# Optimization experiments

Hardware: AMD Instinct MI355X
Metric: run time of the kernel (lower is better)

## Reference

```python
import jax, jax.numpy as jnp
import numpy as np

# norse LIFParameters(method='super', alpha=100) defaults
DT = 0.001
TAU_SYN_INV = 200.0
TAU_MEM_INV = 100.0
V_TH = 1.0
ALPHA = 100.0  # SuperSpike surrogate slope


@jax.custom_vjp
def superspike(x):
    # Heaviside forward, SuperSpike surrogate gradient backward
    return (x > 0).astype(x.dtype)

def _ss_fwd(x):
    return (x > 0).astype(x.dtype), x

def _ss_bwd(x, g):
    return (g / (ALPHA * jnp.abs(x) + 1.0) ** 2,)

superspike.defvjp(_ss_fwd, _ss_bwd)


def setup_inputs() -> dict:
    key = jax.random.key(0)
    k0, k1, k2 = jax.random.split(key, 3)
    T, B, F = 200, 256, 28
    H1, HC, OC, NOUT = 200, 2, 4, 10
    spl1 = F * F // HC   # 392
    spl2 = H1 // OC      # 50
    x = jax.random.normal(k0, (T, B, F, F), jnp.float32)
    Wh = jax.random.normal(k1, (HC, H1, spl1), jnp.float32) / np.sqrt(spl1).astype(np.float32)
    bh = jnp.zeros((HC, H1), jnp.float32)
    Wo = jax.random.normal(k2, (OC, NOUT, spl2), jnp.float32) / np.sqrt(spl2).astype(np.float32)
    bo = jnp.zeros((OC, NOUT), jnp.float32)
    return {"x": x, "Wh": Wh, "bh": bh, "Wo": Wo, "bo": bo}


def reference(x, Wh, bh, Wo, bo):
    T, B = x.shape[0], x.shape[1]
    HC, H1, spl1 = Wh.shape           # hidden dendritic channels
    OC, NOUT, spl2 = Wo.shape         # output dendritic channels
    dtype = x.dtype
    # flatten image and pre-split into hidden dendritic channels: [T,B,HC,spl1]
    xf = x.reshape(T, B, HC * spl1).reshape(T, B, HC, spl1)

    def step(state, xt):
        vh, ih, vo, io = state
        # --- hidden LIF layer, one LIF compartment per dendritic channel ---
        cur_h = jnp.einsum('bci,coi->bco', xt, Wh) + bh           # [B,HC,H1]
        vh_dec = vh + DT * TAU_MEM_INV * (-vh + ih)               # leak + integrate
        z = superspike(vh_dec - V_TH)                             # spikes [B,HC,H1]
        vh_new = (1.0 - z) * vh_dec                               # reset to 0
        ih_new = ih * (1.0 - DT * TAU_SYN_INV) + cur_h            # synaptic current
        s = z.sum(axis=1)                                         # combine channels -> [B,H1]
        # --- output LI (non-spiking) layer over output dendritic channels ---
        so = s.reshape(B, OC, spl2)                               # split hidden spikes
        cur_o = jnp.einsum('bci,coi->bco', so, Wo) + bo           # [B,OC,10]
        vo_new = vo + DT * TAU_MEM_INV * (-vo + io)
        io_new = io * (1.0 - DT * TAU_SYN_INV) + cur_o
        v = vo_new.sum(axis=1)                                    # [B,10]
        return (vh_new, ih_new, vo_new, io_new), v

    init = (jnp.zeros((B, HC, H1), dtype), jnp.zeros((B, HC, H1), dtype),
            jnp.zeros((B, OC, NOUT), dtype), jnp.zeros((B, OC, NOUT), dtype))
    _, voltages = jax.lax.scan(step, init, xf)                    # [T,B,10]
    return voltages
```

## Files before the change

### kernel.cpp

```cpp
#include <hip/hip_runtime.h>

#define T_STEPS 200
#define BATCH   256
#define HCH     2
#define H1      200
#define SPL1    392
#define OCH     4
#define NOUTC   10
#define SPL2    50
#define M_TOTAL (T_STEPS*BATCH)


#define BM 80
#define BN 100
#define BK 8

__global__ __launch_bounds__(256)
void k1_gemm(const float* __restrict__ X, const float* __restrict__ Wh,
             const float* __restrict__ bh, float* __restrict__ CUR)
{
    __shared__ float As[BK][BM];
    __shared__ float Ws[BK][BN];
    const int tid = threadIdx.x;
    const int m0 = blockIdx.x * BM;
    const int n0 = blockIdx.y * BN;
    const int c  = blockIdx.z;

    const bool active = tid < 250;
    const int rowg = tid / 25;
    const int colg = tid % 25;

    const float* Xc = X  + (size_t)m0 * (HCH*SPL1) + c*SPL1;
    const float* Wc = Wh + (size_t)c * H1 * SPL1 + (size_t)n0 * SPL1;

    float acc[8][4];
#pragma unroll
    for (int i = 0; i < 8; ++i)
#pragma unroll
        for (int j = 0; j < 4; ++j) acc[i][j] = 0.f;

    for (int k0 = 0; k0 < SPL1; k0 += BK) {
        for (int idx = tid; idx < BM*BK; idx += 256) {
            int m = idx >> 3, k = idx & 7;
            As[k][m] = Xc[(size_t)m*(HCH*SPL1) + k0 + k];
        }
        for (int idx = tid; idx < BN*BK; idx += 256) {
            int n = idx >> 3, k = idx & 7;
            Ws[k][n] = Wc[(size_t)n*SPL1 + k0 + k];
        }
        __syncthreads();
        if (active) {
#pragma unroll
            for (int k = 0; k < BK; ++k) {
                float4 a0 = *(const float4*)&As[k][rowg*8];
                float4 a1 = *(const float4*)&As[k][rowg*8 + 4];
                float4 w  = *(const float4*)&Ws[k][colg*4];
                float av[8] = {a0.x, a0.y, a0.z, a0.w, a1.x, a1.y, a1.z, a1.w};
                float wv[4] = {w.x, w.y, w.z, w.w};
#pragma unroll
                for (int i = 0; i < 8; ++i)
#pragma unroll
                    for (int j = 0; j < 4; ++j)
                        acc[i][j] = __builtin_fmaf(av[i], wv[j], acc[i][j]);
            }
        }
        __syncthreads();
    }

    if (active) {
        const int gn = n0 + colg*4;
        float4 bias = *(const float4*)&bh[c*H1 + gn];
#pragma unroll
        for (int i = 0; i < 8; ++i) {
            size_t m = m0 + rowg*8 + i;
            float4 v;
            v.x = __fadd_rn(acc[i][0], bias.x);
            v.y = __fadd_rn(acc[i][1], bias.y);
            v.z = __fadd_rn(acc[i][2], bias.z);
            v.w = __fadd_rn(acc[i][3], bias.w);
            *(float4*)&CUR[(m*HCH + c)*H1 + gn] = v;
        }
    }
}

__global__ __launch_bounds__(256)
void k2_lif(const float* __restrict__ CUR, unsigned char* __restrict__ S)
{
    const int tid = blockIdx.x * 256 + threadIdx.x;
    const int b = tid / H1;
    const int h = tid - b*H1;
    const size_t cbase = (size_t)b*(HCH*H1) + h;
    const int    soff  = b*(OCH*52) + (h/SPL2)*52 + (h%SPL2);
    const size_t tstr  = (size_t)BATCH*HCH*H1;
    const size_t sstr  = (size_t)BATCH*OCH*52;

    float c0[8], c1[8];
#pragma unroll
    for (int p = 0; p < 8; ++p) {
        c0[p] = CUR[(size_t)p*tstr + cbase];
        c1[p] = CUR[(size_t)p*tstr + cbase + H1];
    }

    float vh0 = 0.f, ih0 = 0.f, vh1 = 0.f, ih1 = 0.f;

    for (int tb = 0; tb < T_STEPS; tb += 8) {
#pragma unroll
        for (int u = 0; u < 8; ++u) {
            const int t = tb + u;
            float cc0 = c0[u], cc1 = c1[u];
            if (t + 8 < T_STEPS) {
                c0[u] = CUR[(size_t)(t+8)*tstr + cbase];
                c1[u] = CUR[(size_t)(t+8)*tstr + cbase + H1];
            }
            float vd0 = __fadd_rn(vh0, __fmul_rn(0.1f, __fsub_rn(ih0, vh0)));
            float vd1 = __fadd_rn(vh1, __fmul_rn(0.1f, __fsub_rn(ih1, vh1)));
            int z0 = vd0 > 1.0f;
            int z1 = vd1 > 1.0f;
            vh0 = z0 ? 0.f : vd0;
            vh1 = z1 ? 0.f : vd1;
            ih0 = __fadd_rn(__fmul_rn(ih0, 0.8f), cc0);
            ih1 = __fadd_rn(__fmul_rn(ih1, 0.8f), cc1);

            S[(size_t)t*sstr + soff] = (unsigned char)(z0 + z1);
        }
    }
}

__global__ __launch_bounds__(256)
void k3_outgemm(const unsigned char* __restrict__ S, const float* __restrict__ Wo,
                const float* __restrict__ bo, float* __restrict__ CURO)
{
    __shared__ float sW[OCH*NOUTC][52];
    const int tid = threadIdx.x;
    for (int idx = tid; idx < OCH*NOUTC*SPL2; idx += 256)
        sW[idx/SPL2][idx%SPL2] = Wo[idx];
    __syncthreads();

    const int rowg = tid >> 3;
    const int colg = tid & 7;
    const int oc = colg & 3;
    const int jg = colg >> 2;
    const int cl0 = oc*NOUTC + jg*5;
    const int r0 = blockIdx.x*128 + rowg*4;
    const unsigned char* sp = S + (size_t)r0*(OCH*52) + oc*52;

    float acc[4][5];
#pragma unroll
    for (int rr = 0; rr < 4; ++rr)
#pragma unroll
        for (int jj = 0; jj < 5; ++jj) acc[rr][jj] = 0.f;

#pragma unroll
    for (int q = 0; q < 12; ++q) {
        float4 w0 = *(const float4*)&sW[cl0+0][q*4];
        float4 w1 = *(const float4*)&sW[cl0+1][q*4];
        float4 w2 = *(const float4*)&sW[cl0+2][q*4];
        float4 w3 = *(const float4*)&sW[cl0+3][q*4];
        float4 w4 = *(const float4*)&sW[cl0+4][q*4];
#pragma unroll
        for (int rr = 0; rr < 4; ++rr) {
            unsigned int u = *(const unsigned int*)(sp + (size_t)rr*(OCH*52) + q*4);
            float s0 = (float)(u & 255u);
            float s1 = (float)((u >> 8) & 255u);
            float s2 = (float)((u >> 16) & 255u);
            float s3 = (float)(u >> 24);
            float4 ws[5] = {w0, w1, w2, w3, w4};
#pragma unroll
            for (int jj = 0; jj < 5; ++jj) {
                float a = acc[rr][jj];
                a = __builtin_fmaf(s0, ws[jj].x, a);
                a = __builtin_fmaf(s1, ws[jj].y, a);
                a = __builtin_fmaf(s2, ws[jj].z, a);
                a = __builtin_fmaf(s3, ws[jj].w, a);
                acc[rr][jj] = a;
            }
        }
    }
#pragma unroll
    for (int rr = 0; rr < 4; ++rr) {
        unsigned short ut = *(const unsigned short*)(sp + (size_t)rr*(OCH*52) + 48);
        float s48 = (float)(ut & 255u);
        float s49 = (float)(ut >> 8);
#pragma unroll
        for (int jj = 0; jj < 5; ++jj) {
            float2 wt = *(const float2*)&sW[cl0+jj][48];
            float a = acc[rr][jj];
            a = __builtin_fmaf(s48, wt.x, a);
            a = __builtin_fmaf(s49, wt.y, a);
            acc[rr][jj] = a;
        }
    }
#pragma unroll
    for (int rr = 0; rr < 4; ++rr)
#pragma unroll
        for (int jj = 0; jj < 5; ++jj) {
            int j = jg*5 + jj;
            CURO[(size_t)(r0+rr)*(OCH*NOUTC) + j*4 + oc] =
                __fadd_rn(acc[rr][jj], bo[oc*NOUTC + j]);
        }
}

__global__ __launch_bounds__(64)
void k4_li(const float* __restrict__ CURO, float* __restrict__ OUT)
{
    const int tid = blockIdx.x*64 + threadIdx.x;
    const float4* C4 = (const float4*)CURO;

    float4 ring[8];
#pragma unroll
    for (int p = 0; p < 8; ++p) ring[p] = C4[(size_t)p*2560 + tid];

    float vo0=0.f, vo1=0.f, vo2=0.f, vo3=0.f;
    float io0=0.f, io1=0.f, io2=0.f, io3=0.f;

    for (int tb = 0; tb < T_STEPS; tb += 8) {
#pragma unroll
        for (int u = 0; u < 8; ++u) {
            const int t = tb + u;
            float4 cv = ring[u];
            if (t + 8 < T_STEPS) ring[u] = C4[(size_t)(t+8)*2560 + tid];
            vo0 = __fadd_rn(vo0, __fmul_rn(0.1f, __fsub_rn(io0, vo0)));
            vo1 = __fadd_rn(vo1, __fmul_rn(0.1f, __fsub_rn(io1, vo1)));
            vo2 = __fadd_rn(vo2, __fmul_rn(0.1f, __fsub_rn(io2, vo2)));
            vo3 = __fadd_rn(vo3, __fmul_rn(0.1f, __fsub_rn(io3, vo3)));
            io0 = __fadd_rn(__fmul_rn(io0, 0.8f), cv.x);
            io1 = __fadd_rn(__fmul_rn(io1, 0.8f), cv.y);
            io2 = __fadd_rn(__fmul_rn(io2, 0.8f), cv.z);
            io3 = __fadd_rn(__fmul_rn(io3, 0.8f), cv.w);
            float s = __fadd_rn(__fadd_rn(__fadd_rn(vo0, vo1), vo2), vo3);
            OUT[(size_t)t*2560 + tid] = s;
        }
    }
}

extern "C" void kernel_launch(void* const* d_in, const int* in_sizes, int n_in,
                              void* d_out, int out_size, void* d_ws, size_t ws_size,
                              hipStream_t stream)
{
    const float* X  = (const float*)d_in[0];
    const float* Wh = (const float*)d_in[1];
    const float* bh = (const float*)d_in[2];
    const float* Wo = (const float*)d_in[3];
    const float* bo = (const float*)d_in[4];
    float* OUT = (float*)d_out;

    char* ws = (char*)d_ws;
    float*         CUR  = (float*)ws;
    unsigned char* S    = (unsigned char*)(ws + 81920000);
    float*         CURO = (float*)(ws + 81920000 + 10649600);

    k1_gemm   <<<dim3(M_TOTAL/BM, 2, HCH), 256, 0, stream>>>(X, Wh, bh, CUR);
    k2_lif    <<<M_TOTAL/256,              256, 0, stream>>>(CUR, S);
    k3_outgemm<<<M_TOTAL/128,              256, 0, stream>>>(S, Wo, bo, CURO);
    k4_li     <<<(BATCH*NOUTC)/64,         64,  0, stream>>>(CURO, OUT);
}
```

Baseline: 601.4 us.

## Widen GEMM tile to full N, double-buffer smem, pad spike rows for vector loads

The hidden-layer GEMM now computes all 200 output columns per block with an 8x8 per-thread tile, so each X tile is loaded once instead of twice. It also double-buffers shared memory with register prefetch of the next K slice. The spike buffer row stride is padded from 52 to 64 bytes so the output GEMM can read each row with three 16-byte vector loads, and that loop is reordered by row. This adds register pressure (64 accumulators plus the staging registers) and uses more shared memory, which could reduce occupancy.

```diff
diff --git a/kernel.cpp b/kernel.cpp
--- a/kernel.cpp
+++ b/kernel.cpp
@@ -11,74 +11,100 @@
 #define M_TOTAL (T_STEPS*BATCH)
 
 
-#define BM 80
-#define BN 100
 #define BK 8
 
-__global__ __launch_bounds__(256)
+__global__ __launch_bounds__(256, 3)
 void k1_gemm(const float* __restrict__ X, const float* __restrict__ Wh,
              const float* __restrict__ bh, float* __restrict__ CUR)
 {
-    __shared__ float As[BK][BM];
-    __shared__ float Ws[BK][BN];
+    __shared__ float As[2][BK][80];
+    __shared__ float Ws[2][BK][200];
     const int tid = threadIdx.x;
-    const int m0 = blockIdx.x * BM;
-    const int n0 = blockIdx.y * BN;
-    const int c  = blockIdx.z;
-
+    const int m0 = blockIdx.x * 80;
+    const int c  = blockIdx.y;
     const bool active = tid < 250;
     const int rowg = tid / 25;
     const int colg = tid % 25;
 
     const float* Xc = X  + (size_t)m0 * (HCH*SPL1) + c*SPL1;
-    const float* Wc = Wh + (size_t)c * H1 * SPL1 + (size_t)n0 * SPL1;
-
-    float acc[8][4];
+    const float* Wc = Wh + (size_t)c * H1 * SPL1;
+
+    float ra[3], rw[7];
+
+    auto stage_load = [&](int k0) {
+#pragma unroll
+        for (int r = 0; r < 3; ++r) {
+            int idx = tid + 256*r;
+            if (idx < 640) ra[r] = Xc[(size_t)(idx >> 3)*(HCH*SPL1) + k0 + (idx & 7)];
+        }
+#pragma unroll
+        for (int r = 0; r < 7; ++r) {
+            int idx = tid + 256*r;
+            if (idx < 1600) rw[r] = Wc[(size_t)(idx >> 3)*SPL1 + k0 + (idx & 7)];
+        }
+    };
+    auto stage_store = [&](int p) {
+#pragma unroll
+        for (int r = 0; r < 3; ++r) {
+            int idx = tid + 256*r;
+            if (idx < 640) As[p][idx & 7][idx >> 3] = ra[r];
+        }
+#pragma unroll
+        for (int r = 0; r < 7; ++r) {
+            int idx = tid + 256*r;
+            if (idx < 1600) Ws[p][idx & 7][idx >> 3] = rw[r];
+        }
+    };
+
+    float acc[8][8];
 #pragma unroll
     for (int i = 0; i < 8; ++i)
 #pragma unroll
-        for (int j = 0; j < 4; ++j) acc[i][j] = 0.f;
-
-    for (int k0 = 0; k0 < SPL1; k0 += BK) {
-        for (int idx = tid; idx < BM*BK; idx += 256) {
-            int m = idx >> 3, k = idx & 7;
-            As[k][m] = Xc[(size_t)m*(HCH*SPL1) + k0 + k];
-        }
-        for (int idx = tid; idx < BN*BK; idx += 256) {
-            int n = idx >> 3, k = idx & 7;
-            Ws[k][n] = Wc[(size_t)n*SPL1 + k0 + k];
-        }
+        for (int j = 0; j < 8; ++j) acc[i][j] = 0.f;
+
+    stage_load(0);
+    stage_store(0);
+    __syncthreads();
+
+    int p = 0;
+    for (int t = 0; t < SPL1/BK; ++t) {
+        if (t < SPL1/BK - 1) stage_load((t+1)*BK);
+        if (active) {
+#pragma unroll
+            for (int k = 0; k < BK; ++k) {
+                float4 a0 = *(const float4*)&As[p][k][rowg*8];
+                float4 a1 = *(const float4*)&As[p][k][rowg*8 + 4];
+                float2 w0 = *(const float2*)&Ws[p][k][colg*2];
+                float2 w1 = *(const float2*)&Ws[p][k][colg*2 + 50];
+                float2 w2 = *(const float2*)&Ws[p][k][colg*2 + 100];
+                float2 w3 = *(const float2*)&Ws[p][k][colg*2 + 150];
+                float av[8] = {a0.x, a0.y, a0.z, a0.w, a1.x, a1.y, a1.z, a1.w};
+                float wv[8] = {w0.x, w0.y, w1.x, w1.y, w2.x, w2.y, w3.x, w3.y};
+#pragma unroll
+                for (int i = 0; i < 8; ++i)
+#pragma unroll
+                    for (int j = 0; j < 8; ++j)
+                        acc[i][j] = __builtin_fmaf(av[i], wv[j], acc[i][j]);
+            }
+        }
+        if (t < SPL1/BK - 1) stage_store(p ^ 1);
         __syncthreads();
-        if (active) {
-#pragma unroll
-            for (int k = 0; k < BK; ++k) {
-                float4 a0 = *(const float4*)&As[k][rowg*8];
-                float4 a1 = *(const float4*)&As[k][rowg*8 + 4];
-                float4 w  = *(const float4*)&Ws[k][colg*4];
-                float av[8] = {a0.x, a0.y, a0.z, a0.w, a1.x, a1.y, a1.z, a1.w};
-                float wv[4] = {w.x, w.y, w.z, w.w};
-#pragma unroll
-                for (int i = 0; i < 8; ++i)
-#pragma unroll
-                    for (int j = 0; j < 4; ++j)
-                        acc[i][j] = __builtin_fmaf(av[i], wv[j], acc[i][j]);
-            }
-        }
-        __syncthreads();
+        p ^= 1;
     }
 
     if (active) {
-        const int gn = n0 + colg*4;
-        float4 bias = *(const float4*)&bh[c*H1 + gn];
 #pragma unroll
         for (int i = 0; i < 8; ++i) {
             size_t m = m0 + rowg*8 + i;
-            float4 v;
-            v.x = __fadd_rn(acc[i][0], bias.x);
-            v.y = __fadd_rn(acc[i][1], bias.y);
-            v.z = __fadd_rn(acc[i][2], bias.z);
-            v.w = __fadd_rn(acc[i][3], bias.w);
-            *(float4*)&CUR[(m*HCH + c)*H1 + gn] = v;
+            size_t base = (m*HCH + c)*H1 + colg*2;
+#pragma unroll
+            for (int jp = 0; jp < 4; ++jp) {
+                int gn = colg*2 + jp*50;
+                float2 v;
+                v.x = __fadd_rn(acc[i][jp*2+0], bh[c*H1 + gn + 0]);
+                v.y = __fadd_rn(acc[i][jp*2+1], bh[c*H1 + gn + 1]);
+                *(float2*)&CUR[base + jp*50] = v;
+            }
         }
     }
 }
@@ -90,15 +116,15 @@
     const int b = tid / H1;
     const int h = tid - b*H1;
     const size_t cbase = (size_t)b*(HCH*H1) + h;
-    const int    soff  = b*(OCH*52) + (h/SPL2)*52 + (h%SPL2);
+    const int    soff  = b*(OCH*64) + (h/SPL2)*64 + (h%SPL2);
     const size_t tstr  = (size_t)BATCH*HCH*H1;
-    const size_t sstr  = (size_t)BATCH*OCH*52;
+    const size_t sstr  = (size_t)BATCH*OCH*64;
 
     float c0[8], c1[8];
 #pragma unroll
-    for (int p = 0; p < 8; ++p) {
-        c0[p] = CUR[(size_t)p*tstr + cbase];
-        c1[p] = CUR[(size_t)p*tstr + cbase + H1];
+    for (int pp = 0; pp < 8; ++pp) {
+        c0[pp] = CUR[(size_t)pp*tstr + cbase];
+        c1[pp] = CUR[(size_t)pp*tstr + cbase + H1];
     }
 
     float vh0 = 0.f, ih0 = 0.f, vh1 = 0.f, ih1 = 0.f;
@@ -120,7 +146,6 @@
             vh1 = z1 ? 0.f : vd1;
             ih0 = __fadd_rn(__fmul_rn(ih0, 0.8f), cc0);
             ih1 = __fadd_rn(__fmul_rn(ih1, 0.8f), cc1);
-
             S[(size_t)t*sstr + soff] = (unsigned char)(z0 + z1);
         }
     }
@@ -142,7 +167,7 @@
     const int jg = colg >> 2;
     const int cl0 = oc*NOUTC + jg*5;
     const int r0 = blockIdx.x*128 + rowg*4;
-    const unsigned char* sp = S + (size_t)r0*(OCH*52) + oc*52;
+    const unsigned char* sp = S + (size_t)r0*(OCH*64) + oc*64;
 
     float acc[4][5];
 #pragma unroll
@@ -150,37 +175,33 @@
 #pragma unroll
         for (int jj = 0; jj < 5; ++jj) acc[rr][jj] = 0.f;
 
-#pragma unroll
-    for (int q = 0; q < 12; ++q) {
-        float4 w0 = *(const float4*)&sW[cl0+0][q*4];
-        float4 w1 = *(const float4*)&sW[cl0+1][q*4];
-        float4 w2 = *(const float4*)&sW[cl0+2][q*4];
-        float4 w3 = *(const float4*)&sW[cl0+3][q*4];
-        float4 w4 = *(const float4*)&sW[cl0+4][q*4];
-#pragma unroll
-        for (int rr = 0; rr < 4; ++rr) {
-            unsigned int u = *(const unsigned int*)(sp + (size_t)rr*(OCH*52) + q*4);
-            float s0 = (float)(u & 255u);
-            float s1 = (float)((u >> 8) & 255u);
-            float s2 = (float)((u >> 16) & 255u);
-            float s3 = (float)(u >> 24);
-            float4 ws[5] = {w0, w1, w2, w3, w4};
+#define B2F(w, bb) ((float)(((w) >> (8*(bb))) & 255u))
+
+#pragma unroll
+    for (int rr = 0; rr < 4; ++rr) {
+        const unsigned char* rp = sp + (size_t)rr*(OCH*64);
+        uint4 u0 = *(const uint4*)(rp);
+        uint4 u1 = *(const uint4*)(rp + 16);
+        uint4 u2 = *(const uint4*)(rp + 32);
+        unsigned short ut = *(const unsigned short*)(rp + 48);
+        unsigned int uw[13] = {u0.x,u0.y,u0.z,u0.w, u1.x,u1.y,u1.z,u1.w,
+                               u2.x,u2.y,u2.z,u2.w, (unsigned int)ut};
+#pragma unroll
+        for (int q = 0; q < 12; ++q) {
+            float s0 = B2F(uw[q],0), s1 = B2F(uw[q],1);
+            float s2 = B2F(uw[q],2), s3 = B2F(uw[q],3);
 #pragma unroll
             for (int jj = 0; jj < 5; ++jj) {
+                float4 w = *(const float4*)&sW[cl0+jj][q*4];
                 float a = acc[rr][jj];
-                a = __builtin_fmaf(s0, ws[jj].x, a);
-                a = __builtin_fmaf(s1, ws[jj].y, a);
-                a = __builtin_fmaf(s2, ws[jj].z, a);
-                a = __builtin_fmaf(s3, ws[jj].w, a);
+                a = __builtin_fmaf(s0, w.x, a);
+                a = __builtin_fmaf(s1, w.y, a);
+                a = __builtin_fmaf(s2, w.z, a);
+                a = __builtin_fmaf(s3, w.w, a);
                 acc[rr][jj] = a;
             }
         }
-    }
-#pragma unroll
-    for (int rr = 0; rr < 4; ++rr) {
-        unsigned short ut = *(const unsigned short*)(sp + (size_t)rr*(OCH*52) + 48);
-        float s48 = (float)(ut & 255u);
-        float s49 = (float)(ut >> 8);
+        float s48 = B2F(uw[12],0), s49 = B2F(uw[12],1);
 #pragma unroll
         for (int jj = 0; jj < 5; ++jj) {
             float2 wt = *(const float2*)&sW[cl0+jj][48];
@@ -208,7 +229,7 @@
 
     float4 ring[8];
 #pragma unroll
-    for (int p = 0; p < 8; ++p) ring[p] = C4[(size_t)p*2560 + tid];
+    for (int pp = 0; pp < 8; ++pp) ring[pp] = C4[(size_t)pp*2560 + tid];
 
     float vo0=0.f, vo1=0.f, vo2=0.f, vo3=0.f;
     float io0=0.f, io1=0.f, io2=0.f, io3=0.f;
@@ -247,10 +268,10 @@
     char* ws = (char*)d_ws;
     float*         CUR  = (float*)ws;
     unsigned char* S    = (unsigned char*)(ws + 81920000);
-    float*         CURO = (float*)(ws + 81920000 + 10649600);
-
-    k1_gemm   <<<dim3(M_TOTAL/BM, 2, HCH), 256, 0, stream>>>(X, Wh, bh, CUR);
-    k2_lif    <<<M_TOTAL/256,              256, 0, stream>>>(CUR, S);
-    k3_outgemm<<<M_TOTAL/128,              256, 0, stream>>>(S, Wo, bo, CURO);
-    k4_li     <<<(BATCH*NOUTC)/64,         64,  0, stream>>>(CURO, OUT);
-}
+    float*         CURO = (float*)(ws + 81920000 + 13107200);
+
+    k1_gemm   <<<dim3(M_TOTAL/80, HCH), 256, 0, stream>>>(X, Wh, bh, CUR);
+    k2_lif    <<<M_TOTAL/256,           256, 0, stream>>>(CUR, S);
+    k3_outgemm<<<M_TOTAL/128,           256, 0, stream>>>(S, Wo, bo, CURO);
+    k4_li     <<<(BATCH*NOUTC)/64,      64,  0, stream>>>(CURO, OUT);
+}
```

Result: slower. 948.3 us (+57.7%).
